# Performance work log

Measured on AMD Instinct MI355X. Metric: run time of the kernel, lower is better.

The kernel has to match this reference:

```python
import jax, jax.numpy as jnp
import numpy as np

N = 50000        # number of nodes
E = 1600000      # number of (directed) edges, ~degree 32
D = 128          # latent_dim
L = 2            # num_layers
NEG_SLOPE = 0.01 # torch F.leaky_relu default


def setup_inputs() -> dict:
    key = jax.random.key(0)
    k1, k2, k3, k4 = jax.random.split(key, 4)
    h = jax.random.normal(k1, (N, D), dtype=jnp.float32)
    src = jax.random.randint(k2, (E,), 0, N, dtype=jnp.int32)
    dst = jax.random.randint(k3, (E,), 0, N, dtype=jnp.int32)
    # attn_fc per layer: Linear(2*D, 1, bias=False) -> weight vector of length 2*D
    att_w = jax.random.normal(k4, (L, 2 * D), dtype=jnp.float32) * 0.1
    return {"h": h, "src": src, "dst": dst, "att_w": att_w}


def _segment_softmax(e, seg, n):
    # numerically-stable softmax over edges grouped by destination node
    m = jax.ops.segment_max(e, seg, num_segments=n)      # [N]
    ex = jnp.exp(e - m[seg])                             # [E]
    s = jax.ops.segment_sum(ex, seg, num_segments=n)     # [N]
    return ex / s[seg]


def reference(h, src, dst, att_w):
    n, d = h.shape
    for l in range(att_w.shape[0]):
        w_src = att_w[l, :d]   # weight applied to edges.src['h']
        w_dst = att_w[l, d:]   # weight applied to edges.dst['h']
        # a = attn_fc(concat(h_src, h_dst)) = h_src @ w_src + h_dst @ w_dst
        a = h[src] @ w_src + h[dst] @ w_dst               # [E]
        e = jnp.where(a > 0, a, NEG_SLOPE * a)            # leaky_relu
        alpha = _segment_softmax(e, dst, n)               # edge_softmax by dst
        # update_all: m = h_src * e ; h_dst = sum(m)
        h = jax.ops.segment_sum(h[src] * alpha[:, None], dst, num_segments=n)
    return h
```

## Files before the change

### kernel.cpp

```cpp
#include <hip/hip_runtime.h>
#include <hip/hip_fp16.h>
#include <math.h>

#define NEG_SLOPE 0.01f
#define BKT_BITS 7
#define BKT_MASK 127
#define SBLOCKS  256
#define STPB     512


__global__ void bkhist_kernel(const int* __restrict__ dst, int* __restrict__ blockhist,
                              int E, int NB, int chunk) {
    extern __shared__ int lh[];
    for (int k = threadIdx.x; k < NB; k += blockDim.x) lh[k] = 0;
    __syncthreads();
    int b = blockIdx.x;
    int beg = b * chunk, end = min(E, beg + chunk);
    for (int e = beg + (int)threadIdx.x; e < end; e += blockDim.x)
        atomicAdd(&lh[dst[e] >> BKT_BITS], 1);
    __syncthreads();
    for (int k = threadIdx.x; k < NB; k += blockDim.x)
        blockhist[k * SBLOCKS + b] = lh[k];
}

__global__ void scan1_kernel(const int* __restrict__ in, int* __restrict__ local_excl,
                             int* __restrict__ partials, int n) {
    __shared__ int sm[1024];
    int i = blockIdx.x * 1024 + threadIdx.x;
    int x = (i < n) ? in[i] : 0;
    sm[threadIdx.x] = x;
    __syncthreads();
    for (int off = 1; off < 1024; off <<= 1) {
        int y = (threadIdx.x >= (unsigned)off) ? sm[threadIdx.x - off] : 0;
        __syncthreads();
        sm[threadIdx.x] += y;
        __syncthreads();
    }
    if (i < n) local_excl[i] = sm[threadIdx.x] - x;
    if (threadIdx.x == 1023) partials[blockIdx.x] = sm[1023];
}

__global__ void scan2_kernel(int* __restrict__ partials, int nchunks) {
    __shared__ int sm[1024];
    int x = (threadIdx.x < (unsigned)nchunks) ? partials[threadIdx.x] : 0;
    sm[threadIdx.x] = x;
    __syncthreads();
    for (int off = 1; off < 1024; off <<= 1) {
        int y = (threadIdx.x >= (unsigned)off) ? sm[threadIdx.x - off] : 0;
        __syncthreads();
        sm[threadIdx.x] += y;
        __syncthreads();
    }
    partials[threadIdx.x] = sm[threadIdx.x] - x;
    if (threadIdx.x == 1023) partials[1024] = sm[1023];
}

__global__ void scan3_kernel(const int* __restrict__ local_excl, const int* __restrict__ partials,
                             int* __restrict__ out, int n) {
    int i = blockIdx.x * 1024 + threadIdx.x;
    if (i < n) out[i] = local_excl[i] + partials[blockIdx.x];
    if (i == n) out[n] = partials[1024];
}

__global__ void bksplit_kernel(const int* __restrict__ src, const int* __restrict__ dst,
                               const int* __restrict__ bh_scan, unsigned* __restrict__ pairs,
                               int E, int NB, int chunk) {
    extern __shared__ int lm[];
    int* lbase = lm;
    int* lcnt  = lm + NB;
    int b = blockIdx.x;
    for (int k = threadIdx.x; k < NB; k += blockDim.x) {
        lbase[k] = bh_scan[k * SBLOCKS + b];
        lcnt[k]  = 0;
    }
    __syncthreads();
    int beg = b * chunk, end = min(E, beg + chunk);
    for (int e = beg + (int)threadIdx.x; e < end; e += blockDim.x) {
        int d = dst[e];
        int k = d >> BKT_BITS;
        int pos = lbase[k] + atomicAdd(&lcnt[k], 1);
        pairs[pos] = ((unsigned)src[e] << BKT_BITS) | (unsigned)(d & BKT_MASK);
    }
}

__global__ void csr_build_kernel(const unsigned* __restrict__ pairs, const int* __restrict__ bh_scan,
                                 int* __restrict__ row_ptr, int* __restrict__ csr_src,
                                 int E, int N, int NB) {
    __shared__ int ldeg[128];
    __shared__ int lscan[128];
    __shared__ int lpos[128];
    int k = blockIdx.x;
    int bbase = bh_scan[k * SBLOCKS];
    int bend  = bh_scan[(k + 1) * SBLOCKS];
    if (threadIdx.x < 128) ldeg[threadIdx.x] = 0;
    __syncthreads();
    for (int i = bbase + (int)threadIdx.x; i < bend; i += blockDim.x)
        atomicAdd(&ldeg[pairs[i] & BKT_MASK], 1);
    __syncthreads();
    int x = (threadIdx.x < 128) ? ldeg[threadIdx.x] : 0;
    if (threadIdx.x < 128) lscan[threadIdx.x] = x;
    __syncthreads();
    for (int off = 1; off < 128; off <<= 1) {
        int y = 0;
        if (threadIdx.x < 128 && threadIdx.x >= (unsigned)off) y = lscan[threadIdx.x - off];
        __syncthreads();
        if (threadIdx.x < 128) lscan[threadIdx.x] += y;
        __syncthreads();
    }
    if (threadIdx.x < 128) {
        int excl = lscan[threadIdx.x] - x;
        int node = (k << BKT_BITS) + threadIdx.x;
        if (node < N) row_ptr[node] = bbase + excl;
        lpos[threadIdx.x] = excl;
    }
    if (k == NB - 1 && threadIdx.x == 0) row_ptr[N] = E;
    __syncthreads();
    for (int i = bbase + (int)threadIdx.x; i < bend; i += blockDim.x) {
        unsigned p = pairs[i];
        int pos = atomicAdd(&lpos[p & BKT_MASK], 1);
        csr_src[bbase + pos] = (int)(p >> BKT_BITS);
    }
}


__global__ void stconv_kernel(const float* __restrict__ h, const float* __restrict__ att_w_l,
                              float* __restrict__ s, float* __restrict__ t,
                              __half* __restrict__ h16, int n) {
    int gid  = blockIdx.x * blockDim.x + threadIdx.x;
    int v    = gid >> 6;
    int lane = threadIdx.x & 63;
    if (v >= n) return;
    float2 hv = ((const float2*)(h + (size_t)v * 128))[lane];
    ((__half2*)(h16 + (size_t)v * 128))[lane] = __floats2half2_rn(hv.x, hv.y);
    float2 ws = ((const float2*)att_w_l)[lane];
    float2 wd = ((const float2*)(att_w_l + 128))[lane];
    float ps = hv.x * ws.x + hv.y * ws.y;
    float pt = hv.x * wd.x + hv.y * wd.y;
    for (int off = 32; off > 0; off >>= 1) {
        ps += __shfl_down(ps, off);
        pt += __shfl_down(pt, off);
    }
    if (lane == 0) { s[v] = ps; t[v] = pt; }
}

__device__ __forceinline__ void gath(const __half* __restrict__ hin, int uu, float wgt,
                                     int hlane, float4& acc) {
    float2 r = ((const float2*)(hin + (size_t)uu * 128))[hlane];
    float2 f01 = __half22float2(*(const __half2*)&r.x);
    float2 f23 = __half22float2(*(const __half2*)&r.y);
    acc.x = fmaf(wgt, f01.x, acc.x); acc.y = fmaf(wgt, f01.y, acc.y);
    acc.z = fmaf(wgt, f23.x, acc.z); acc.w = fmaf(wgt, f23.y, acc.w);
}

template<bool LAST>
__global__ void agg_kernel(const __half* __restrict__ hin, const float* __restrict__ s,
                           const float* __restrict__ t, const int* __restrict__ row_ptr,
                           const int* __restrict__ csr_src,
                           __half* __restrict__ hout16, float* __restrict__ outf,
                           const float* __restrict__ att_w_next,
                           float* __restrict__ s2, float* __restrict__ t2, int n) {
    int gid   = blockIdx.x * blockDim.x + threadIdx.x;
    int v     = gid >> 6;
    int lane  = threadIdx.x & 63;
    if (v >= n) return;
    int half  = lane >> 5;
    int hlane = lane & 31;

    int beg = row_ptr[v];
    int end = row_ptr[v + 1];
    float tv = t[v];

    float4 acc = make_float4(0.f, 0.f, 0.f, 0.f);
    float lsum_l = 0.f;

    for (int base = beg; base < end; base += 64) {
        int cnt = end - base;
        if (cnt > 64) cnt = 64;
        int idx = base + min(lane, cnt - 1);
        int u   = csr_src[idx];
        float a = s[u] + tv;
        float e = (a > 0.f) ? a : NEG_SLOPE * a;
        float wl = (lane < cnt) ? __expf(e) : 0.f;
        lsum_l += wl;
        int steps = (cnt + 1) >> 1;
        int k = 0;
        for (; k + 1 < steps; k += 2) {
            int sl0 = (k << 1) + half;
            int sl1 = (k << 1) + 2 + half;
            int   u0 = __shfl(u, sl0);
            float w0 = __shfl(wl, sl0);
            int   u1 = __shfl(u, sl1);
            float w1 = __shfl(wl, sl1);
            gath(hin, u0, w0, hlane, acc);
            gath(hin, u1, w1, hlane, acc);
        }
        if (k < steps) {
            int sl = (k << 1) + half;
            int   u0 = __shfl(u, sl);
            float w0 = __shfl(wl, sl);
            gath(hin, u0, w0, hlane, acc);
        }
    }
    float lsum = lsum_l;
    for (int off = 32; off > 0; off >>= 1) lsum += __shfl_xor(lsum, off);
    acc.x += __shfl_xor(acc.x, 32);
    acc.y += __shfl_xor(acc.y, 32);
    acc.z += __shfl_xor(acc.z, 32);
    acc.w += __shfl_xor(acc.w, 32);
    float inv_l = (lsum > 0.f) ? (1.0f / lsum) : 0.f;
    acc.x *= inv_l; acc.y *= inv_l; acc.z *= inv_l; acc.w *= inv_l;

    if (LAST) {
        if (half == 0)
            ((float4*)(outf + (size_t)v * 128))[hlane] = acc;
    } else {
        if (half == 0) {
            __half2 q01 = __floats2half2_rn(acc.x, acc.y);
            __half2 q23 = __floats2half2_rn(acc.z, acc.w);
            float2 packed;
            packed.x = *(const float*)&q01;
            packed.y = *(const float*)&q23;
            ((float2*)(hout16 + (size_t)v * 128))[hlane] = packed;
        }
        float4 ws4 = ((const float4*)att_w_next)[hlane];
        float4 wd4 = ((const float4*)(att_w_next + 128))[hlane];
        float ps = acc.x * ws4.x + acc.y * ws4.y + acc.z * ws4.z + acc.w * ws4.w;
        float pt = acc.x * wd4.x + acc.y * wd4.y + acc.z * wd4.z + acc.w * wd4.w;
        for (int off = 16; off > 0; off >>= 1) {
            ps += __shfl_down(ps, off);
            pt += __shfl_down(pt, off);
        }
        if (lane == 0) { s2[v] = ps; t2[v] = pt; }
    }
}


extern "C" void kernel_launch(void* const* d_in, const int* in_sizes, int n_in,
                              void* d_out, int out_size, void* d_ws, size_t ws_size,
                              hipStream_t stream) {
    const float* h0    = (const float*)d_in[0];
    const int*   src   = (const int*)d_in[1];
    const int*   dst   = (const int*)d_in[2];
    const float* att_w = (const float*)d_in[3];
    int N = in_sizes[0] / 128;
    int E = in_sizes[1];
    int L = in_sizes[3] / 256;
    float* out = (float*)d_out;

    int NB = (N + BKT_MASK) >> BKT_BITS;
    int n2 = NB * SBLOCKS;
    int chunk = (E + SBLOCKS - 1) / SBLOCKS;
    int nch2 = (n2 + 1023) / 1024;

    char* ws = (char*)d_ws;
    size_t off = 0;
    auto alloc = [&](size_t bytes) -> void* {
        void* p = ws + off;
        off = (off + bytes + 511) & ~(size_t)511;
        return p;
    };
    int*      row_ptr   = (int*)     alloc((size_t)(N + 1) * 4);
    int*      csr_src   = (int*)     alloc((size_t)E * 4);
    float*    s1        = (float*)   alloc((size_t)N * 4);
    float*    t1        = (float*)   alloc((size_t)N * 4);
    float*    s2        = (float*)   alloc((size_t)N * 4);
    float*    t2        = (float*)   alloc((size_t)N * 4);
    __half*   hA        = (__half*)  alloc((size_t)N * 128 * 2);
    __half*   hB        = (__half*)  alloc((size_t)N * 128 * 2);
    unsigned* pairs     = (unsigned*)alloc((size_t)E * 4);
    int*      blockhist = (int*)     alloc((size_t)n2 * 4);
    int*      bh_scan   = (int*)     alloc((size_t)(n2 + 1) * 4);
    int*      local_ex  = (int*)     alloc((size_t)n2 * 4);
    int*      partials  = (int*)     alloc(1025 * 4);

    bkhist_kernel<<<SBLOCKS, STPB, NB * 4, stream>>>(dst, blockhist, E, NB, chunk);
    scan1_kernel<<<nch2, 1024, 0, stream>>>(blockhist, local_ex, partials, n2);
    scan2_kernel<<<1, 1024, 0, stream>>>(partials, nch2);
    scan3_kernel<<<nch2, 1024, 0, stream>>>(local_ex, partials, bh_scan, n2);
    bksplit_kernel<<<SBLOCKS, STPB, 2 * NB * 4, stream>>>(src, dst, bh_scan, pairs, E, NB, chunk);
    csr_build_kernel<<<NB, 512, 0, stream>>>(pairs, bh_scan, row_ptr, csr_src, E, N, NB);

    const int tb = 256;
    int node_blocks = (N * 64 + tb - 1) / tb;

    stconv_kernel<<<node_blocks, tb, 0, stream>>>(h0, att_w, s1, t1, hA, N);

    __half* hin = hA;
    __half* hnx = hB;
    float *sc = s1, *tc = t1, *sn = s2, *tn = t2;
    for (int l = 0; l < L; ++l) {
        if (l == L - 1) {
            agg_kernel<true><<<node_blocks, tb, 0, stream>>>(
                hin, sc, tc, row_ptr, csr_src, nullptr, out, nullptr, nullptr, nullptr, N);
        } else {
            agg_kernel<false><<<node_blocks, tb, 0, stream>>>(
                hin, sc, tc, row_ptr, csr_src, hnx, nullptr,
                att_w + (size_t)(l + 1) * 256, sn, tn, N);
            __half* tmp = hin; hin = hnx; hnx = tmp;
            float* tf;
            tf = sc; sc = sn; sn = tf;
            tf = tc; tc = tn; tn = tf;
        }
    }
}
```

Baseline: 238.2 us.

## Fuse CSR build and projection into one cooperative kernel; two nodes per wavefront

```diff
diff --git a/kernel.cpp b/kernel.cpp
--- a/kernel.cpp
+++ b/kernel.cpp
@@ -1,151 +1,152 @@
 #include <hip/hip_runtime.h>
 #include <hip/hip_fp16.h>
+#include <hip/hip_cooperative_groups.h>
 #include <math.h>
 
 #define NEG_SLOPE 0.01f
 #define BKT_BITS 7
 #define BKT_MASK 127
-#define SBLOCKS  256
-#define STPB     512
-
-
-__global__ void bkhist_kernel(const int* __restrict__ dst, int* __restrict__ blockhist,
-                              int E, int NB, int chunk) {
-    extern __shared__ int lh[];
-    for (int k = threadIdx.x; k < NB; k += blockDim.x) lh[k] = 0;
+#define PG 256
+#define PT 512
+
+
+struct PrepArgs {
+    const int* dst; const int* src; const float* h0; const float* att_w;
+    int* blockhist; int* local_ex; int* partials; int* bh_scan;
+    unsigned* pairs; int* row_ptr; int* csr_src;
+    float* s1; float* t1; __half* hA;
+    int N, E, NB, chunk, n2, nch;
+};
+
+__global__ void __launch_bounds__(PT) prep_coop(PrepArgs A) {
+    cooperative_groups::grid_group grid = cooperative_groups::this_grid();
+    __shared__ int smem[1024];
+    int b = blockIdx.x, tid = threadIdx.x;
+
+    {
+        int lane = tid & 63;
+        int wv = b * (PT / 64) + (tid >> 6);
+        for (int v = wv; v < A.N; v += PG * (PT / 64)) {
+            float2 hv = ((const float2*)(A.h0 + (size_t)v * 128))[lane];
+            ((__half2*)(A.hA + (size_t)v * 128))[lane] = __floats2half2_rn(hv.x, hv.y);
+            float2 wsv = ((const float2*)A.att_w)[lane];
+            float2 wdv = ((const float2*)(A.att_w + 128))[lane];
+            float ps = hv.x * wsv.x + hv.y * wsv.y;
+            float pt = hv.x * wdv.x + hv.y * wdv.y;
+            for (int off = 32; off > 0; off >>= 1) {
+                ps += __shfl_down(ps, off);
+                pt += __shfl_down(pt, off);
+            }
+            if (lane == 0) { A.s1[v] = ps; A.t1[v] = pt; }
+        }
+    }
+    for (int k = tid; k < A.NB; k += PT) smem[k] = 0;
     __syncthreads();
-    int b = blockIdx.x;
-    int beg = b * chunk, end = min(E, beg + chunk);
-    for (int e = beg + (int)threadIdx.x; e < end; e += blockDim.x)
-        atomicAdd(&lh[dst[e] >> BKT_BITS], 1);
+    {
+        int beg = b * A.chunk, endq = min(A.E, beg + A.chunk);
+        for (int e = beg + tid; e < endq; e += PT)
+            atomicAdd(&smem[A.dst[e] >> BKT_BITS], 1);
+    }
     __syncthreads();
-    for (int k = threadIdx.x; k < NB; k += blockDim.x)
-        blockhist[k * SBLOCKS + b] = lh[k];
+    for (int k = tid; k < A.NB; k += PT) A.blockhist[k * PG + b] = smem[k];
+    grid.sync();
+
+    if (b < A.nch) {
+        int i = b * PT + tid;
+        int x = (i < A.n2) ? A.blockhist[i] : 0;
+        smem[tid] = x;
+        __syncthreads();
+        for (int off = 1; off < PT; off <<= 1) {
+            int y = (tid >= off) ? smem[tid - off] : 0;
+            __syncthreads();
+            smem[tid] += y;
+            __syncthreads();
+        }
+        if (i < A.n2) A.local_ex[i] = smem[tid] - x;
+        if (tid == PT - 1) A.partials[b] = smem[PT - 1];
+    }
+    grid.sync();
+
+    if (b == 0) {
+        int x = (tid < A.nch) ? A.partials[tid] : 0;
+        smem[tid] = x;
+        __syncthreads();
+        for (int off = 1; off < PT; off <<= 1) {
+            int y = (tid >= off) ? smem[tid - off] : 0;
+            __syncthreads();
+            smem[tid] += y;
+            __syncthreads();
+        }
+        if (tid < A.nch) A.partials[tid] = smem[tid] - x;
+        if (tid == PT - 1) A.partials[A.nch] = smem[PT - 1];
+    }
+    grid.sync();
+
+    for (int i = b * PT + tid; i < A.n2; i += PG * PT)
+        A.bh_scan[i] = A.local_ex[i] + A.partials[i >> 9];
+    if (b == 0 && tid == 0) A.bh_scan[A.n2] = A.partials[A.nch];
+    grid.sync();
+
+    {
+        int* lbase = smem;
+        int* lcnt  = smem + A.NB;
+        for (int k = tid; k < A.NB; k += PT) {
+            lbase[k] = A.bh_scan[k * PG + b];
+            lcnt[k]  = 0;
+        }
+        __syncthreads();
+        int beg = b * A.chunk, endq = min(A.E, beg + A.chunk);
+        for (int e = beg + tid; e < endq; e += PT) {
+            int d = A.dst[e];
+            int k = d >> BKT_BITS;
+            int pos = lbase[k] + atomicAdd(&lcnt[k], 1);
+            A.pairs[pos] = ((unsigned)A.src[e] << BKT_BITS) | (unsigned)(d & BKT_MASK);
+        }
+    }
+    grid.sync();
+
+    for (int k = b; k < A.NB; k += PG) {
+        int* ldeg  = smem;
+        int* lscan = smem + 128;
+        int* lpos  = smem + 256;
+        int bbase = A.bh_scan[k * PG];
+        int bend  = A.bh_scan[(k + 1) * PG];
+        __syncthreads();
+        if (tid < 128) ldeg[tid] = 0;
+        __syncthreads();
+        for (int i = bbase + tid; i < bend; i += PT)
+            atomicAdd(&ldeg[A.pairs[i] & BKT_MASK], 1);
+        __syncthreads();
+        int x = (tid < 128) ? ldeg[tid] : 0;
+        if (tid < 128) lscan[tid] = x;
+        __syncthreads();
+        for (int off = 1; off < 128; off <<= 1) {
+            int y = 0;
+            if (tid < 128 && tid >= off) y = lscan[tid - off];
+            __syncthreads();
+            if (tid < 128) lscan[tid] += y;
+            __syncthreads();
+        }
+        if (tid < 128) {
+            int excl = lscan[tid] - x;
+            int node = (k << BKT_BITS) + tid;
+            if (node < A.N) A.row_ptr[node] = bbase + excl;
+            lpos[tid] = excl;
+        }
+        __syncthreads();
+        for (int i = bbase + tid; i < bend; i += PT) {
+            unsigned p = A.pairs[i];
+            int pos = atomicAdd(&lpos[p & BKT_MASK], 1);
+            A.csr_src[bbase + pos] = (int)(p >> BKT_BITS);
+        }
+    }
+    if (b == 0 && tid == 0) A.row_ptr[A.N] = A.E;
 }
 
-__global__ void scan1_kernel(const int* __restrict__ in, int* __restrict__ local_excl,
-                             int* __restrict__ partials, int n) {
-    __shared__ int sm[1024];
-    int i = blockIdx.x * 1024 + threadIdx.x;
-    int x = (i < n) ? in[i] : 0;
-    sm[threadIdx.x] = x;
-    __syncthreads();
-    for (int off = 1; off < 1024; off <<= 1) {
-        int y = (threadIdx.x >= (unsigned)off) ? sm[threadIdx.x - off] : 0;
-        __syncthreads();
-        sm[threadIdx.x] += y;
-        __syncthreads();
-    }
-    if (i < n) local_excl[i] = sm[threadIdx.x] - x;
-    if (threadIdx.x == 1023) partials[blockIdx.x] = sm[1023];
-}
-
-__global__ void scan2_kernel(int* __restrict__ partials, int nchunks) {
-    __shared__ int sm[1024];
-    int x = (threadIdx.x < (unsigned)nchunks) ? partials[threadIdx.x] : 0;
-    sm[threadIdx.x] = x;
-    __syncthreads();
-    for (int off = 1; off < 1024; off <<= 1) {
-        int y = (threadIdx.x >= (unsigned)off) ? sm[threadIdx.x - off] : 0;
-        __syncthreads();
-        sm[threadIdx.x] += y;
-        __syncthreads();
-    }
-    partials[threadIdx.x] = sm[threadIdx.x] - x;
-    if (threadIdx.x == 1023) partials[1024] = sm[1023];
-}
-
-__global__ void scan3_kernel(const int* __restrict__ local_excl, const int* __restrict__ partials,
-                             int* __restrict__ out, int n) {
-    int i = blockIdx.x * 1024 + threadIdx.x;
-    if (i < n) out[i] = local_excl[i] + partials[blockIdx.x];
-    if (i == n) out[n] = partials[1024];
-}
-
-__global__ void bksplit_kernel(const int* __restrict__ src, const int* __restrict__ dst,
-                               const int* __restrict__ bh_scan, unsigned* __restrict__ pairs,
-                               int E, int NB, int chunk) {
-    extern __shared__ int lm[];
-    int* lbase = lm;
-    int* lcnt  = lm + NB;
-    int b = blockIdx.x;
-    for (int k = threadIdx.x; k < NB; k += blockDim.x) {
-        lbase[k] = bh_scan[k * SBLOCKS + b];
-        lcnt[k]  = 0;
-    }
-    __syncthreads();
-    int beg = b * chunk, end = min(E, beg + chunk);
-    for (int e = beg + (int)threadIdx.x; e < end; e += blockDim.x) {
-        int d = dst[e];
-        int k = d >> BKT_BITS;
-        int pos = lbase[k] + atomicAdd(&lcnt[k], 1);
-        pairs[pos] = ((unsigned)src[e] << BKT_BITS) | (unsigned)(d & BKT_MASK);
-    }
-}
-
-__global__ void csr_build_kernel(const unsigned* __restrict__ pairs, const int* __restrict__ bh_scan,
-                                 int* __restrict__ row_ptr, int* __restrict__ csr_src,
-                                 int E, int N, int NB) {
-    __shared__ int ldeg[128];
-    __shared__ int lscan[128];
-    __shared__ int lpos[128];
-    int k = blockIdx.x;
-    int bbase = bh_scan[k * SBLOCKS];
-    int bend  = bh_scan[(k + 1) * SBLOCKS];
-    if (threadIdx.x < 128) ldeg[threadIdx.x] = 0;
-    __syncthreads();
-    for (int i = bbase + (int)threadIdx.x; i < bend; i += blockDim.x)
-        atomicAdd(&ldeg[pairs[i] & BKT_MASK], 1);
-    __syncthreads();
-    int x = (threadIdx.x < 128) ? ldeg[threadIdx.x] : 0;
-    if (threadIdx.x < 128) lscan[threadIdx.x] = x;
-    __syncthreads();
-    for (int off = 1; off < 128; off <<= 1) {
-        int y = 0;
-        if (threadIdx.x < 128 && threadIdx.x >= (unsigned)off) y = lscan[threadIdx.x - off];
-        __syncthreads();
-        if (threadIdx.x < 128) lscan[threadIdx.x] += y;
-        __syncthreads();
-    }
-    if (threadIdx.x < 128) {
-        int excl = lscan[threadIdx.x] - x;
-        int node = (k << BKT_BITS) + threadIdx.x;
-        if (node < N) row_ptr[node] = bbase + excl;
-        lpos[threadIdx.x] = excl;
-    }
-    if (k == NB - 1 && threadIdx.x == 0) row_ptr[N] = E;
-    __syncthreads();
-    for (int i = bbase + (int)threadIdx.x; i < bend; i += blockDim.x) {
-        unsigned p = pairs[i];
-        int pos = atomicAdd(&lpos[p & BKT_MASK], 1);
-        csr_src[bbase + pos] = (int)(p >> BKT_BITS);
-    }
-}
-
-
-__global__ void stconv_kernel(const float* __restrict__ h, const float* __restrict__ att_w_l,
-                              float* __restrict__ s, float* __restrict__ t,
-                              __half* __restrict__ h16, int n) {
-    int gid  = blockIdx.x * blockDim.x + threadIdx.x;
-    int v    = gid >> 6;
-    int lane = threadIdx.x & 63;
-    if (v >= n) return;
-    float2 hv = ((const float2*)(h + (size_t)v * 128))[lane];
-    ((__half2*)(h16 + (size_t)v * 128))[lane] = __floats2half2_rn(hv.x, hv.y);
-    float2 ws = ((const float2*)att_w_l)[lane];
-    float2 wd = ((const float2*)(att_w_l + 128))[lane];
-    float ps = hv.x * ws.x + hv.y * ws.y;
-    float pt = hv.x * wd.x + hv.y * wd.y;
-    for (int off = 32; off > 0; off >>= 1) {
-        ps += __shfl_down(ps, off);
-        pt += __shfl_down(pt, off);
-    }
-    if (lane == 0) { s[v] = ps; t[v] = pt; }
-}
 
 __device__ __forceinline__ void gath(const __half* __restrict__ hin, int uu, float wgt,
-                                     int hlane, float4& acc) {
-    float2 r = ((const float2*)(hin + (size_t)uu * 128))[hlane];
+                                     int sub, float4& acc) {
+    float2 r = ((const float2*)(hin + (size_t)uu * 128))[sub];
     float2 f01 = __half22float2(*(const __half2*)&r.x);
     float2 f23 = __half22float2(*(const __half2*)&r.y);
     acc.x = fmaf(wgt, f01.x, acc.x); acc.y = fmaf(wgt, f01.y, acc.y);
@@ -155,82 +156,79 @@
 template<bool LAST>
 __global__ void agg_kernel(const __half* __restrict__ hin, const float* __restrict__ s,
                            const float* __restrict__ t, const int* __restrict__ row_ptr,
-                           const int* __restrict__ csr_src,
+                           const int* __restrict__ csr_src, int E,
                            __half* __restrict__ hout16, float* __restrict__ outf,
                            const float* __restrict__ att_w_next,
                            float* __restrict__ s2, float* __restrict__ t2, int n) {
     int gid   = blockIdx.x * blockDim.x + threadIdx.x;
-    int v     = gid >> 6;
     int lane  = threadIdx.x & 63;
-    if (v >= n) return;
     int half  = lane >> 5;
-    int hlane = lane & 31;
-
-    int beg = row_ptr[v];
-    int end = row_ptr[v + 1];
-    float tv = t[v];
+    int sub   = lane & 31;
+    int v     = (gid >> 6) * 2 + half;
+    bool valid = (v < n);
+    int vc    = valid ? v : (n - 1);
+    int beg = row_ptr[vc];
+    int end = row_ptr[vc + 1];
+    if (!valid) end = beg;
+    float tv = t[vc];
+
+    int tiles = (end - beg + 31) >> 5;
+    tiles = max(tiles, __shfl_xor(tiles, 32));
 
     float4 acc = make_float4(0.f, 0.f, 0.f, 0.f);
-    float lsum_l = 0.f;
-
-    for (int base = beg; base < end; base += 64) {
+    float lsum = 0.f;
+    int hbase = half << 5;
+    for (int j = 0; j < tiles; ++j) {
+        int base = beg + (j << 5);
         int cnt = end - base;
-        if (cnt > 64) cnt = 64;
-        int idx = base + min(lane, cnt - 1);
-        int u   = csr_src[idx];
+        cnt = min(max(cnt, 0), 32);
+        int idx = base + min(sub, max(cnt - 1, 0));
+        idx = min(idx, E - 1);
+        int u = csr_src[idx];
         float a = s[u] + tv;
         float e = (a > 0.f) ? a : NEG_SLOPE * a;
-        float wl = (lane < cnt) ? __expf(e) : 0.f;
-        lsum_l += wl;
-        int steps = (cnt + 1) >> 1;
+        float wl = (sub < cnt) ? __expf(e) : 0.f;
+        lsum += wl;
+        int kmax = max(cnt, __shfl_xor(cnt, 32));
         int k = 0;
-        for (; k + 1 < steps; k += 2) {
-            int sl0 = (k << 1) + half;
-            int sl1 = (k << 1) + 2 + half;
-            int   u0 = __shfl(u, sl0);
-            float w0 = __shfl(wl, sl0);
-            int   u1 = __shfl(u, sl1);
-            float w1 = __shfl(wl, sl1);
-            gath(hin, u0, w0, hlane, acc);
-            gath(hin, u1, w1, hlane, acc);
-        }
-        if (k < steps) {
-            int sl = (k << 1) + half;
-            int   u0 = __shfl(u, sl);
-            float w0 = __shfl(wl, sl);
-            gath(hin, u0, w0, hlane, acc);
-        }
-    }
-    float lsum = lsum_l;
-    for (int off = 32; off > 0; off >>= 1) lsum += __shfl_xor(lsum, off);
-    acc.x += __shfl_xor(acc.x, 32);
-    acc.y += __shfl_xor(acc.y, 32);
-    acc.z += __shfl_xor(acc.z, 32);
-    acc.w += __shfl_xor(acc.w, 32);
+        for (; k + 1 < kmax; k += 2) {
+            int   u0 = __shfl(u,  hbase + k);
+            float w0 = __shfl(wl, hbase + k);
+            int   u1 = __shfl(u,  hbase + k + 1);
+            float w1 = __shfl(wl, hbase + k + 1);
+            gath(hin, u0, w0, sub, acc);
+            gath(hin, u1, w1, sub, acc);
+        }
+        if (k < kmax) {
+            int   u0 = __shfl(u,  hbase + k);
+            float w0 = __shfl(wl, hbase + k);
+            gath(hin, u0, w0, sub, acc);
+        }
+    }
+    for (int off = 16; off > 0; off >>= 1) lsum += __shfl_xor(lsum, off);
     float inv_l = (lsum > 0.f) ? (1.0f / lsum) : 0.f;
     acc.x *= inv_l; acc.y *= inv_l; acc.z *= inv_l; acc.w *= inv_l;
 
     if (LAST) {
-        if (half == 0)
-            ((float4*)(outf + (size_t)v * 128))[hlane] = acc;
+        if (valid) ((float4*)(outf + (size_t)v * 128))[sub] = acc;
     } else {
-        if (half == 0) {
+        if (valid) {
             __half2 q01 = __floats2half2_rn(acc.x, acc.y);
             __half2 q23 = __floats2half2_rn(acc.z, acc.w);
             float2 packed;
             packed.x = *(const float*)&q01;
             packed.y = *(const float*)&q23;
-            ((float2*)(hout16 + (size_t)v * 128))[hlane] = packed;
-        }
-        float4 ws4 = ((const float4*)att_w_next)[hlane];
-        float4 wd4 = ((const float4*)(att_w_next + 128))[hlane];
+            ((float2*)(hout16 + (size_t)v * 128))[sub] = packed;
+        }
+        float4 ws4 = ((const float4*)att_w_next)[sub];
+        float4 wd4 = ((const float4*)(att_w_next + 128))[sub];
         float ps = acc.x * ws4.x + acc.y * ws4.y + acc.z * ws4.z + acc.w * ws4.w;
         float pt = acc.x * wd4.x + acc.y * wd4.y + acc.z * wd4.z + acc.w * wd4.w;
         for (int off = 16; off > 0; off >>= 1) {
-            ps += __shfl_down(ps, off);
-            pt += __shfl_down(pt, off);
-        }
-        if (lane == 0) { s2[v] = ps; t2[v] = pt; }
+            ps += __shfl_xor(ps, off);
+            pt += __shfl_xor(pt, off);
+        }
+        if (valid && sub == 0) { s2[v] = ps; t2[v] = pt; }
     }
 }
 
@@ -248,9 +246,9 @@
     float* out = (float*)d_out;
 
     int NB = (N + BKT_MASK) >> BKT_BITS;
-    int n2 = NB * SBLOCKS;
-    int chunk = (E + SBLOCKS - 1) / SBLOCKS;
-    int nch2 = (n2 + 1023) / 1024;
+    int n2 = NB * PG;
+    int chunk = (E + PG - 1) / PG;
+    int nch = (n2 + PT - 1) / PT;
 
     char* ws = (char*)d_ws;
     size_t off = 0;
@@ -273,17 +271,18 @@
     int*      local_ex  = (int*)     alloc((size_t)n2 * 4);
     int*      partials  = (int*)     alloc(1025 * 4);
 
-    bkhist_kernel<<<SBLOCKS, STPB, NB * 4, stream>>>(dst, blockhist, E, NB, chunk);
-    scan1_kernel<<<nch2, 1024, 0, stream>>>(blockhist, local_ex, partials, n2);
-    scan2_kernel<<<1, 1024, 0, stream>>>(partials, nch2);
-    scan3_kernel<<<nch2, 1024, 0, stream>>>(local_ex, partials, bh_scan, n2);
-    bksplit_kernel<<<SBLOCKS, STPB, 2 * NB * 4, stream>>>(src, dst, bh_scan, pairs, E, NB, chunk);
-    csr_build_kernel<<<NB, 512, 0, stream>>>(pairs, bh_scan, row_ptr, csr_src, E, N, NB);
+    PrepArgs A;
+    A.dst = dst; A.src = src; A.h0 = h0; A.att_w = att_w;
+    A.blockhist = blockhist; A.local_ex = local_ex; A.partials = partials;
+    A.bh_scan = bh_scan; A.pairs = pairs; A.row_ptr = row_ptr; A.csr_src = csr_src;
+    A.s1 = s1; A.t1 = t1; A.hA = hA;
+    A.N = N; A.E = E; A.NB = NB; A.chunk = chunk; A.n2 = n2; A.nch = nch;
+    void* kargs[] = { &A };
+    hipLaunchCooperativeKernel((void*)prep_coop, dim3(PG), dim3(PT), kargs, 0, stream);
 
     const int tb = 256;
-    int node_blocks = (N * 64 + tb - 1) / tb;
-
-    stconv_kernel<<<node_blocks, tb, 0, stream>>>(h0, att_w, s1, t1, hA, N);
+    int npairs = (N + 1) / 2;
+    int node_blocks = (npairs * 64 + tb - 1) / tb;
 
     __half* hin = hA;
     __half* hnx = hB;
@@ -291,10 +290,10 @@
     for (int l = 0; l < L; ++l) {
         if (l == L - 1) {
             agg_kernel<true><<<node_blocks, tb, 0, stream>>>(
-                hin, sc, tc, row_ptr, csr_src, nullptr, out, nullptr, nullptr, nullptr, N);
+                hin, sc, tc, row_ptr, csr_src, E, nullptr, out, nullptr, nullptr, nullptr, N);
         } else {
             agg_kernel<false><<<node_blocks, tb, 0, stream>>>(
-                hin, sc, tc, row_ptr, csr_src, hnx, nullptr,
+                hin, sc, tc, row_ptr, csr_src, E, hnx, nullptr,
                 att_w + (size_t)(l + 1) * 256, sn, tn, N);
             __half* tmp = hin; hin = hnx; hnx = tmp;
             float* tf;
```

Measured after the change: 420.2 us. 1.76x slower.
